# Performance work log

Hardware: AMD Instinct MI355X
Metric: run time of the kernel (lower is better)

## Reference

```python
import jax, jax.numpy as jnp
import numpy as np
from jax import lax

D_MODEL = 192; PATCH = 16; CH = 3
D_INNER = 384; D_STATE = 16; D_CONV = 4; DT_RANK = 12  # mamba_ssm defaults: expand=2, dt_rank=ceil(d_model/16)


def setup_inputs() -> dict:
    key = jax.random.key(0)
    ks = jax.random.split(key, 12)
    f32 = jnp.float32
    def rn(k, shape, s=0.02):
        return jax.random.normal(k, shape, f32) * s
    return {
        "x": jax.random.uniform(ks[0], (8, 3, 512, 512), f32),
        "patch_w": rn(ks[1], (D_MODEL, CH, PATCH, PATCH)),
        "patch_b": jnp.zeros((D_MODEL,), f32),
        "in_proj_w": rn(ks[2], (2 * D_INNER, D_MODEL)),
        "conv1d_w": rn(ks[3], (D_INNER, 1, D_CONV)),
        "conv1d_b": jnp.zeros((D_INNER,), f32),
        "x_proj_w": rn(ks[4], (DT_RANK + 2 * D_STATE, D_INNER)),
        "dt_proj_w": rn(ks[5], (D_INNER, DT_RANK)),
        "dt_proj_b": rn(ks[6], (D_INNER,), 0.1),
        "A_log": jnp.log(jnp.broadcast_to(jnp.arange(1, D_STATE + 1, dtype=f32), (D_INNER, D_STATE))),
        "D": jnp.ones((D_INNER,), f32),
        "out_proj_w": rn(ks[7], (D_MODEL, D_INNER)),
        "deconv_w": rn(ks[8], (D_MODEL, 64, PATCH, PATCH)),
        "deconv_b": jnp.zeros((64,), f32),
        "dec_conv_w": rn(ks[9], (CH, 64, 3, 3)),
        "dec_conv_b": jnp.zeros((CH,), f32),
    }


def _mamba(seq, in_proj_w, conv1d_w, conv1d_b, x_proj_w, dt_proj_w, dt_proj_b, A_log, D, out_proj_w):
    # seq: (B, L, d_model)
    B, L, _ = seq.shape
    xz = seq @ in_proj_w.T                              # (B, L, 2*d_inner)
    u, z = jnp.split(xz, 2, axis=-1)
    # depthwise causal conv1d (torch pads d_conv-1 both sides then truncates to L == left-pad only)
    uc = lax.conv_general_dilated(u.transpose(0, 2, 1), conv1d_w, (1,), [(D_CONV - 1, 0)],
                                  dimension_numbers=('NCH', 'OIH', 'NCH'),
                                  feature_group_count=D_INNER)       # (B, d_inner, L)
    u = jax.nn.silu((uc + conv1d_b[:, None]).transpose(0, 2, 1))     # (B, L, d_inner)
    dbc = u @ x_proj_w.T                                              # (B, L, dt_rank + 2*d_state)
    dt, Bm, Cm = jnp.split(dbc, [DT_RANK, DT_RANK + D_STATE], axis=-1)
    delta = jax.nn.softplus(dt @ dt_proj_w.T + dt_proj_b)            # (B, L, d_inner)
    A = -jnp.exp(A_log)                                               # (d_inner, d_state)
    dA = jnp.exp(delta[..., None] * A)                                # (B, L, d_inner, d_state)
    dBu = delta[..., None] * Bm[:, :, None, :] * u[..., None]         # (B, L, d_inner, d_state)
    def step(h, inp):
        a, b = inp
        h = a * h + b
        return h, h
    h0 = jnp.zeros((B, D_INNER, D_STATE), seq.dtype)
    _, hs = lax.scan(step, h0, (dA.transpose(1, 0, 2, 3), dBu.transpose(1, 0, 2, 3)))
    y = jnp.einsum('lbdn,bln->bld', hs, Cm) + u * D                   # (B, L, d_inner)
    y = y * jax.nn.silu(z)
    return y @ out_proj_w.T                                           # (B, L, d_model)


def reference(x, patch_w, patch_b, in_proj_w, conv1d_w, conv1d_b, x_proj_w,
              dt_proj_w, dt_proj_b, A_log, D, out_proj_w,
              deconv_w, deconv_b, dec_conv_w, dec_conv_b):
    B = x.shape[0]
    e = lax.conv_general_dilated(x, patch_w, (PATCH, PATCH), 'VALID',
                                 dimension_numbers=('NCHW', 'OIHW', 'NCHW')) + patch_b[:, None, None]
    h, w = e.shape[2], e.shape[3]
    seq = e.reshape(B, D_MODEL, h * w).transpose(0, 2, 1)             # (B, L, d_model)
    seq = _mamba(seq, in_proj_w, conv1d_w, conv1d_b, x_proj_w, dt_proj_w, dt_proj_b, A_log, D, out_proj_w)
    g = seq.transpose(0, 2, 1).reshape(B, D_MODEL, h, w)
    # ConvTranspose2d with stride == kernel_size is a non-overlapping patch expansion
    d = jnp.einsum('bchw,cdpq->bdhpwq', g, deconv_w).reshape(B, 64, h * PATCH, w * PATCH)
    d = jax.nn.relu(d + deconv_b[:, None, None])
    out = lax.conv_general_dilated(d, dec_conv_w, (1, 1), [(1, 1), (1, 1)],
                                   dimension_numbers=('NCHW', 'OIHW', 'NCHW')) + dec_conv_b[:, None, None]
    return jax.nn.sigmoid(out)
```

## Files before the change

kernel.cpp:

```cpp
#include <hip/hip_runtime.h>
#include <math.h>


typedef short bf16x8 __attribute__((ext_vector_type(8)));
typedef float f32x4 __attribute__((ext_vector_type(4)));

__device__ inline unsigned short f2bf(float f) {
    unsigned int u = __float_as_uint(f);
    unsigned int r = (u + 0x7fff + ((u >> 16) & 1)) >> 16;
    return (unsigned short)r;
}
__device__ inline float bf2f(unsigned short s) {
    return __uint_as_float(((unsigned int)s) << 16);
}

__global__ __launch_bounds__(256) void gemm_mfma_flex(
    const unsigned short* __restrict__ A, const unsigned short* __restrict__ W,
    void* __restrict__ Cout, const float* __restrict__ bias,
    int M, int N, int K, int out_bf16)
{
    __shared__ unsigned short As[128][48];
    __shared__ unsigned short Bs[128][48];
    const int tid = threadIdx.x;
    const int wave = tid >> 6, lane = tid & 63;
    const int wm = (wave & 1) * 64, wn = (wave >> 1) * 64;
    const int m0 = blockIdx.y * 128, n0 = blockIdx.x * 128;
    const int quad = lane >> 4, lr = lane & 15;
    const uint4 z4 = {0, 0, 0, 0};

    f32x4 acc[4][4];
    #pragma unroll
    for (int i = 0; i < 4; ++i)
        #pragma unroll
        for (int j = 0; j < 4; ++j)
            acc[i][j] = (f32x4){0.f, 0.f, 0.f, 0.f};

    const int r = tid >> 2, kq = tid & 3;
    for (int k0 = 0; k0 < K; k0 += 32) {
        #pragma unroll
        for (int half = 0; half < 2; ++half) {
            int rr = r + half * 64;
            *(uint4*)(&As[rr][kq * 8]) =
                *(const uint4*)(A + (size_t)(m0 + rr) * K + k0 + kq * 8);
            uint4 bv = z4;
            if (n0 + rr < N)
                bv = *(const uint4*)(W + (size_t)(n0 + rr) * K + k0 + kq * 8);
            *(uint4*)(&Bs[rr][kq * 8]) = bv;
        }
        __syncthreads();
        bf16x8 af[4], bfr[4];
        #pragma unroll
        for (int i = 0; i < 4; ++i) af[i] = *(const bf16x8*)(&As[wm + i * 16 + lr][quad * 8]);
        #pragma unroll
        for (int j = 0; j < 4; ++j) bfr[j] = *(const bf16x8*)(&Bs[wn + j * 16 + lr][quad * 8]);
        #pragma unroll
        for (int i = 0; i < 4; ++i)
            #pragma unroll
            for (int j = 0; j < 4; ++j)
                acc[i][j] = __builtin_amdgcn_mfma_f32_16x16x32_bf16(af[i], bfr[j], acc[i][j], 0, 0, 0);
        __syncthreads();
    }

    #pragma unroll
    for (int i = 0; i < 4; ++i) {
        int gm = m0 + wm + i * 16 + quad * 4;
        #pragma unroll
        for (int j = 0; j < 4; ++j) {
            int gn = n0 + wn + j * 16 + lr;
            if (gn >= N) continue;
            float bv = bias ? bias[gn] : 0.f;
            #pragma unroll
            for (int rr = 0; rr < 4; ++rr) {
                float v = acc[i][j][rr] + bv;
                if (out_bf16) ((unsigned short*)Cout)[(size_t)(gm + rr) * N + gn] = f2bf(v);
                else          ((float*)Cout)[(size_t)(gm + rr) * N + gn] = v;
            }
        }
    }
}

__global__ __launch_bounds__(256) void gemm_xd(
    const unsigned short* __restrict__ A, const unsigned short* __restrict__ W,
    float* __restrict__ delta, float* __restrict__ bc,
    const float* __restrict__ dtb)
{
    __shared__ unsigned short As[128][48];
    __shared__ unsigned short Bs[128][48];
    const int N = 416, K = 384;
    const int tid = threadIdx.x;
    const int wave = tid >> 6, lane = tid & 63;
    const int wm = (wave & 1) * 64, wn = (wave >> 1) * 64;
    const int m0 = blockIdx.y * 128, n0 = blockIdx.x * 128;
    const int quad = lane >> 4, lr = lane & 15;
    const uint4 z4 = {0, 0, 0, 0};

    f32x4 acc[4][4];
    #pragma unroll
    for (int i = 0; i < 4; ++i)
        #pragma unroll
        for (int j = 0; j < 4; ++j)
            acc[i][j] = (f32x4){0.f, 0.f, 0.f, 0.f};

    const int r = tid >> 2, kq = tid & 3;
    for (int k0 = 0; k0 < K; k0 += 32) {
        #pragma unroll
        for (int half = 0; half < 2; ++half) {
            int rr = r + half * 64;
            *(uint4*)(&As[rr][kq * 8]) =
                *(const uint4*)(A + (size_t)(m0 + rr) * K + k0 + kq * 8);
            uint4 bv = z4;
            if (n0 + rr < N)
                bv = *(const uint4*)(W + (size_t)(n0 + rr) * K + k0 + kq * 8);
            *(uint4*)(&Bs[rr][kq * 8]) = bv;
        }
        __syncthreads();
        bf16x8 af[4], bfr[4];
        #pragma unroll
        for (int i = 0; i < 4; ++i) af[i] = *(const bf16x8*)(&As[wm + i * 16 + lr][quad * 8]);
        #pragma unroll
        for (int j = 0; j < 4; ++j) bfr[j] = *(const bf16x8*)(&Bs[wn + j * 16 + lr][quad * 8]);
        #pragma unroll
        for (int i = 0; i < 4; ++i)
            #pragma unroll
            for (int j = 0; j < 4; ++j)
                acc[i][j] = __builtin_amdgcn_mfma_f32_16x16x32_bf16(af[i], bfr[j], acc[i][j], 0, 0, 0);
        __syncthreads();
    }

    #pragma unroll
    for (int i = 0; i < 4; ++i) {
        int gm = m0 + wm + i * 16 + quad * 4;
        #pragma unroll
        for (int j = 0; j < 4; ++j) {
            int gn = n0 + wn + j * 16 + lr;
            if (gn >= N) continue;
            #pragma unroll
            for (int rr = 0; rr < 4; ++rr) {
                float v = acc[i][j][rr];
                if (gn < 384) {
                    v += dtb[gn];
                    v = (v > 20.f) ? v : log1pf(__expf(v));
                    delta[(size_t)(gm + rr) * 384 + gn] = v;
                } else {
                    bc[(size_t)(gm + rr) * 32 + gn - 384] = v;
                }
            }
        }
    }
}

__global__ __launch_bounds__(256) void gemm_mfma_relu_bf16(
    const unsigned short* __restrict__ A0, const unsigned short* __restrict__ W,
    unsigned short* __restrict__ C0, const float* __restrict__ bias, int base_b)
{
    __shared__ unsigned short smem[12288];
    unsigned short* As = smem;
    unsigned short* Bs = smem + 6144;
    const int N = 16384, K = 192;
    const int tid = threadIdx.x;
    const int wave = tid >> 6, lane = tid & 63;
    const int wm = (wave & 1) * 64, wn = (wave >> 1) * 64;
    const int m0 = blockIdx.y * 128, n0 = blockIdx.x * 128;
    const int z = blockIdx.z;
    const unsigned short* A = A0 + (size_t)(base_b + z) * 1024 * 192;
    unsigned short* C = C0 + (size_t)z * 16777216;
    const int quad = lane >> 4, lr = lane & 15;

    f32x4 acc[4][4];
    #pragma unroll
    for (int i = 0; i < 4; ++i)
        #pragma unroll
        for (int j = 0; j < 4; ++j)
            acc[i][j] = (f32x4){0.f, 0.f, 0.f, 0.f};

    const int r = tid >> 2, kq = tid & 3;
    for (int k0 = 0; k0 < K; k0 += 32) {
        #pragma unroll
        for (int half = 0; half < 2; ++half) {
            int rr = r + half * 64;
            *(uint4*)(&As[rr * 48 + kq * 8]) =
                *(const uint4*)(A + (size_t)(m0 + rr) * K + k0 + kq * 8);
            *(uint4*)(&Bs[rr * 48 + kq * 8]) =
                *(const uint4*)(W + (size_t)(n0 + rr) * K + k0 + kq * 8);
        }
        __syncthreads();
        bf16x8 af[4], bfr[4];
        #pragma unroll
        for (int i = 0; i < 4; ++i) af[i] = *(const bf16x8*)(&As[(wm + i * 16 + lr) * 48 + quad * 8]);
        #pragma unroll
        for (int j = 0; j < 4; ++j) bfr[j] = *(const bf16x8*)(&Bs[(wn + j * 16 + lr) * 48 + quad * 8]);
        #pragma unroll
        for (int i = 0; i < 4; ++i)
            #pragma unroll
            for (int j = 0; j < 4; ++j)
                acc[i][j] = __builtin_amdgcn_mfma_f32_16x16x32_bf16(af[i], bfr[j], acc[i][j], 0, 0, 0);
        __syncthreads();
    }

    unsigned short* Ct = smem;
    #pragma unroll
    for (int h = 0; h < 2; ++h) {
        if ((wave & 1) == h) {
            #pragma unroll
            for (int i = 0; i < 4; ++i) {
                int lrow = i * 16 + quad * 4;
                #pragma unroll
                for (int j = 0; j < 4; ++j) {
                    int lcol = wn + j * 16 + lr;
                    float bv = bias[(n0 + lcol) & 63];
                    #pragma unroll
                    for (int rr = 0; rr < 4; ++rr) {
                        float v = fmaxf(acc[i][j][rr] + bv, 0.f);
                        Ct[(lrow + rr) * 136 + lcol] = f2bf(v);
                    }
                }
            }
        }
        __syncthreads();
        #pragma unroll
        for (int p = 0; p < 4; ++p) {
            int idx = p * 256 + tid;
            int row = idx >> 4, cg = idx & 15;
            *(uint4*)(C + (size_t)(m0 + h * 64 + row) * N + n0 + cg * 8) =
                *(const uint4*)(&Ct[row * 136 + cg * 8]);
        }
        __syncthreads();
    }
}

__global__ __launch_bounds__(256) void prep_all(
    const float* __restrict__ x, unsigned short* __restrict__ P,
    const float* __restrict__ patch_w, unsigned short* __restrict__ wp,
    const float* __restrict__ in_proj_w, unsigned short* __restrict__ wi,
    const float* __restrict__ out_proj_w, unsigned short* __restrict__ wo,
    const float* __restrict__ deconv_w, unsigned short* __restrict__ W2,
    const float* __restrict__ dec_conv_w, unsigned short* __restrict__ wconv,
    const float* __restrict__ dtw, const float* __restrict__ xpw,
    unsigned short* __restrict__ wxd)
{
    int i = blockIdx.x * 256 + threadIdx.x;
    if (i < 6291456) {
        int col = i % 768, row = i / 768;
        int b = row >> 10, l = row & 1023;
        int h = l >> 5, w = l & 31;
        int c = col >> 8, p = (col >> 4) & 15, q = col & 15;
        P[i] = f2bf(x[((size_t)(b * 3 + c) * 512 + (h * 16 + p)) * 512 + (w * 16 + q)]);
        return;
    }
    i -= 6291456;
    if (i < 147456) { wp[i] = f2bf(patch_w[i]); return; }
    i -= 147456;
    if (i < 147456) { wi[i] = f2bf(in_proj_w[i]); return; }
    i -= 147456;
    if (i < 73728) { wo[i] = f2bf(out_proj_w[i]); return; }
    i -= 73728;
    if (i < 3145728) {
        int c = i % 192, np = i / 192;
        int k = np & 63, pq = np >> 6;
        W2[i] = f2bf(deconv_w[(size_t)c * 16384 + k * 256 + pq]);
        return;
    }
    i -= 3145728;
    if (i < 9216) {
        int ch = i & 63, m = (i >> 6) & 15, tap = i >> 10;
        int dy = tap / 3, dx = tap % 3;
        float v = (m < 3) ? dec_conv_w[((m * 64 + ch) * 3 + dy) * 3 + dx] : 0.f;
        wconv[i] = f2bf(v);
        return;
    }
    i -= 9216;
    {
        int col = i % 384, row = i / 384;
        float v;
        if (row < 384) {
            v = 0.f;
            #pragma unroll
            for (int j = 0; j < 12; ++j)
                v = fmaf(dtw[row * 12 + j], xpw[j * 384 + col], v);
        } else {
            v = xpw[(row - 384 + 12) * 384 + col];
        }
        wxd[i] = f2bf(v);
    }
}

__global__ __launch_bounds__(256) void conv1d_silu(const unsigned short* __restrict__ xz,
                                                   const float* __restrict__ cw,
                                                   const float* __restrict__ cb,
                                                   float* __restrict__ u32,
                                                   unsigned short* __restrict__ u16)
{
    int idx = blockIdx.x * 256 + threadIdx.x;
    int d = idx % 384;
    int row = idx / 384;
    int l = row & 1023;
    float acc = cb[d];
    #pragma unroll
    for (int j = 0; j < 4; ++j) {
        int ll = l - 3 + j;
        if (ll >= 0) acc += bf2f(xz[(size_t)(row - 3 + j) * 768 + d]) * cw[d * 4 + j];
    }
    float s = acc / (1.f + __expf(-acc));
    u32[idx] = s;
    u16[idx] = f2bf(s);
}

__global__ __launch_bounds__(256) void ssm_pass1(const float* __restrict__ delta,
                                                 const float* __restrict__ bc,
                                                 const float* __restrict__ u,
                                                 const float* __restrict__ A_log,
                                                 float* __restrict__ Pc,
                                                 float* __restrict__ Hc)
{
    const int tid = threadIdx.x;
    const int n4 = tid & 3, dloc = tid >> 2;
    const int c = blockIdx.x, dg = blockIdx.y, b = blockIdx.z;
    const int d = dg * 64 + dloc;
    const int blk = (b * 6 + dg) * 32 + c;
    f32x4 A4 = *(const f32x4*)(A_log + d * 16 + n4 * 4);
    float Aa[4];
    #pragma unroll
    for (int j = 0; j < 4; ++j) Aa[j] = -__expf(A4[j]);
    const float* dp = delta + (size_t)(b * 1024) * 384 + d;
    const float* up = u     + (size_t)(b * 1024) * 384 + d;
    const float* bp = bc    + (size_t)(b * 1024) * 32;
    float P[4] = {1.f, 1.f, 1.f, 1.f}, H[4] = {0.f, 0.f, 0.f, 0.f};
    const int l0 = c * 32;
    for (int l = l0; l < l0 + 32; ++l) {
        float dlv = dp[(size_t)l * 384];
        float ulv = up[(size_t)l * 384];
        f32x4 B4 = *(const f32x4*)(bp + (size_t)l * 32 + n4 * 4);
        float du = dlv * ulv;
        #pragma unroll
        for (int j = 0; j < 4; ++j) {
            float a = __expf(dlv * Aa[j]);
            P[j] *= a;
            H[j] = fmaf(a, H[j], du * B4[j]);
        }
    }
    size_t o = ((size_t)blk * 256 + tid) * 4;
    *(f32x4*)(Pc + o) = (f32x4){P[0], P[1], P[2], P[3]};
    *(f32x4*)(Hc + o) = (f32x4){H[0], H[1], H[2], H[3]};
}

__global__ __launch_bounds__(256) void ssm_pass2(const float* __restrict__ Pc,
                                                 const float* __restrict__ Hc,
                                                 float* __restrict__ h0c)
{
    int t = blockIdx.x * 256 + threadIdx.x;
    int grp = t >> 10, dn = t & 1023;
    float h = 0.f;
    #pragma unroll
    for (int c = 0; c < 32; ++c) {
        size_t idx = ((size_t)(grp * 32 + c)) * 1024 + dn;
        h0c[idx] = h;
        h = fmaf(Pc[idx], h, Hc[idx]);
    }
}

__global__ __launch_bounds__(256) void ssm_pass3(const float* __restrict__ delta,
                                                 const float* __restrict__ bc,
                                                 const float* __restrict__ u,
                                                 const unsigned short* __restrict__ xz,
                                                 const float* __restrict__ A_log,
                                                 const float* __restrict__ Dp,
                                                 const float* __restrict__ h0c,
                                                 unsigned short* __restrict__ y16)
{
    const int tid = threadIdx.x;
    const int n4 = tid & 3, dloc = tid >> 2;
    const int c = blockIdx.x, dg = blockIdx.y, b = blockIdx.z;
    const int d = dg * 64 + dloc;
    const int blk = (b * 6 + dg) * 32 + c;
    f32x4 A4 = *(const f32x4*)(A_log + d * 16 + n4 * 4);
    float Aa[4];
    #pragma unroll
    for (int j = 0; j < 4; ++j) Aa[j] = -__expf(A4[j]);
    float Dv = Dp[d];
    const float* dp = delta + (size_t)(b * 1024) * 384 + d;
    const float* up = u     + (size_t)(b * 1024) * 384 + d;
    const float* bp = bc    + (size_t)(b * 1024) * 32;
    const unsigned short* zp = xz + (size_t)(b * 1024) * 768 + 384 + d;
    unsigned short* yp = y16 + (size_t)(b * 1024) * 384 + d;
    f32x4 h4 = *(const f32x4*)(h0c + ((size_t)blk * 256 + tid) * 4);
    float H[4] = {h4[0], h4[1], h4[2], h4[3]};
    const int l0 = c * 32;
    for (int l = l0; l < l0 + 32; ++l) {
        float dlv = dp[(size_t)l * 384];
        float ulv = up[(size_t)l * 384];
        f32x4 B4 = *(const f32x4*)(bp + (size_t)l * 32 + n4 * 4);
        f32x4 C4 = *(const f32x4*)(bp + (size_t)l * 32 + 16 + n4 * 4);
        float du = dlv * ulv;
        float part = 0.f;
        #pragma unroll
        for (int j = 0; j < 4; ++j) {
            float a = __expf(dlv * Aa[j]);
            H[j] = fmaf(a, H[j], du * B4[j]);
            part = fmaf(H[j], C4[j], part);
        }
        part += __shfl_xor(part, 1, 4);
        part += __shfl_xor(part, 2, 4);
        if (n4 == 0) {
            float z = bf2f(zp[(size_t)l * 768]);
            float sz = z / (1.f + __expf(-z));
            yp[(size_t)l * 384] = f2bf((part + ulv * Dv) * sz);
        }
    }
}

__global__ __launch_bounds__(256) void decconv_mfma(
    const unsigned short* __restrict__ Db, const unsigned short* __restrict__ wconv,
    const float* __restrict__ dcb, float* __restrict__ out, int base_b)
{
    __shared__ unsigned short ds[18 * 18 * 72];
    const int t = threadIdx.x;
    const int pidx = blockIdx.x;
    const int bb = blockIdx.y;
    const int b = base_b + bb;
    const unsigned short* Dbb = Db + (size_t)bb * 16777216;
    const int ph = pidx >> 5, pw = pidx & 31;
    const uint4 z4 = {0, 0, 0, 0};

    const unsigned short* base = Dbb + ((size_t)pidx << 14);
    #pragma unroll
    for (int s = 0; s < 8; ++s) {
        int f = s * 256 + t;
        int k8 = f & 7, pq = f >> 3;
        *(uint4*)&ds[(((pq >> 4) + 1) * 18 + (pq & 15) + 1) * 72 + k8 * 8] =
            *(const uint4*)(base + pq * 64 + k8 * 8);
    }
    {
        int k8 = t & 7, e = (t >> 3) & 15;
        if (t < 128) {
            uint4 v = z4;
            if (ph > 0) v = *(const uint4*)(Dbb + ((size_t)(pidx - 32) << 14) + (240 + e) * 64 + k8 * 8);
            *(uint4*)&ds[(0 * 18 + e + 1) * 72 + k8 * 8] = v;
        } else {
            uint4 v = z4;
            if (ph < 31) v = *(const uint4*)(Dbb + ((size_t)(pidx + 32) << 14) + e * 64 + k8 * 8);
            *(uint4*)&ds[(17 * 18 + e + 1) * 72 + k8 * 8] = v;
        }
        if (t < 128) {
            uint4 v = z4;
            if (pw > 0) v = *(const uint4*)(Dbb + ((size_t)(pidx - 1) << 14) + (e * 16 + 15) * 64 + k8 * 8);
            *(uint4*)&ds[((e + 1) * 18 + 0) * 72 + k8 * 8] = v;
        } else {
            uint4 v = z4;
            if (pw < 31) v = *(const uint4*)(Dbb + ((size_t)(pidx + 1) << 14) + (e * 16) * 64 + k8 * 8);
            *(uint4*)&ds[((e + 1) * 18 + 17) * 72 + k8 * 8] = v;
        }
        if (t < 32) {
            int c = t >> 3;
            int dh = (c >> 1) * 2 - 1, dw = (c & 1) * 2 - 1;
            int nh = ph + dh, nw = pw + dw;
            int sp = dh < 0 ? 15 : 0, sq = dw < 0 ? 15 : 0;
            uint4 v = z4;
            if (nh >= 0 && nh < 32 && nw >= 0 && nw < 32)
                v = *(const uint4*)(Dbb + ((size_t)(nh * 32 + nw) << 14) + (sp * 16 + sq) * 64 + k8 * 8);
            int dy = dh < 0 ? 0 : 17, dx = dw < 0 ? 0 : 17;
            *(uint4*)&ds[(dy * 18 + dx) * 72 + k8 * 8] = v;
        }
    }
    __syncthreads();

    const int wave = t >> 6, lane = t & 63;
    const int quad = lane >> 4, lr = lane & 15;
    f32x4 acc[4];
    #pragma unroll
    for (int i = 0; i < 4; ++i) acc[i] = (f32x4){0.f, 0.f, 0.f, 0.f};

    #pragma unroll
    for (int tap = 0; tap < 9; ++tap) {
        const int dy = tap / 3, dx = tap % 3;
        bf16x8 a0 = *(const bf16x8*)(wconv + (tap * 16 + lr) * 64 + quad * 8);
        bf16x8 a1 = *(const bf16x8*)(wconv + (tap * 16 + lr) * 64 + 32 + quad * 8);
        #pragma unroll
        for (int i = 0; i < 4; ++i) {
            int p = wave * 4 + i;
            const unsigned short* cell = &ds[((p + dy) * 18 + lr + dx) * 72];
            bf16x8 b0 = *(const bf16x8*)(cell + quad * 8);
            bf16x8 b1 = *(const bf16x8*)(cell + 32 + quad * 8);
            acc[i] = __builtin_amdgcn_mfma_f32_16x16x32_bf16(a0, b0, acc[i], 0, 0, 0);
            acc[i] = __builtin_amdgcn_mfma_f32_16x16x32_bf16(a1, b1, acc[i], 0, 0, 0);
        }
    }

    if (quad == 0) {
        float b0 = dcb[0], b1 = dcb[1], b2 = dcb[2];
        #pragma unroll
        for (int i = 0; i < 4; ++i) {
            int Y = ph * 16 + wave * 4 + i, X = pw * 16 + lr;
            size_t o = (size_t)(b * 3) * 262144 + (size_t)Y * 512 + X;
            out[o]          = 1.f / (1.f + __expf(-(acc[i][0] + b0)));
            out[o + 262144] = 1.f / (1.f + __expf(-(acc[i][1] + b1)));
            out[o + 524288] = 1.f / (1.f + __expf(-(acc[i][2] + b2)));
        }
    }
}

#define WS_P16      0
#define WS_DELTA    0
#define WS_SEQ16    3145728
#define WS_XZ16     3538944
#define WS_U32      6684672
#define WS_U16      9830400
#define WS_Y16      9830400
#define WS_BC       10223616
#define WS_PC       10485760
#define WS_HC       12058624
#define WS_H0C      13631488

extern "C" void kernel_launch(void* const* d_in, const int* in_sizes, int n_in,
                              void* d_out, int out_size, void* d_ws, size_t ws_size,
                              hipStream_t stream)
{
    const float* x         = (const float*)d_in[0];
    const float* patch_w   = (const float*)d_in[1];
    const float* patch_b   = (const float*)d_in[2];
    const float* in_proj_w = (const float*)d_in[3];
    const float* conv1d_w  = (const float*)d_in[4];
    const float* conv1d_b  = (const float*)d_in[5];
    const float* x_proj_w  = (const float*)d_in[6];
    const float* dt_proj_w = (const float*)d_in[7];
    const float* dt_proj_b = (const float*)d_in[8];
    const float* A_log     = (const float*)d_in[9];
    const float* Dp        = (const float*)d_in[10];
    const float* out_proj_w= (const float*)d_in[11];
    const float* deconv_w  = (const float*)d_in[12];
    const float* deconv_b  = (const float*)d_in[13];
    const float* dec_conv_w= (const float*)d_in[14];
    const float* dec_conv_b= (const float*)d_in[15];
    float* out = (float*)d_out;
    float* ws  = (float*)d_ws;

    const int G = (ws_size >= (size_t)143157248) ? 4 : 2;
    const size_t wbase = (G == 4) ? 33554432 : 16777216;

    unsigned short* P16   = (unsigned short*)(ws + WS_P16);
    float*          delta = ws + WS_DELTA;
    unsigned short* seq16 = (unsigned short*)(ws + WS_SEQ16);
    unsigned short* xz16  = (unsigned short*)(ws + WS_XZ16);
    float*          u32   = ws + WS_U32;
    unsigned short* u16   = (unsigned short*)(ws + WS_U16);
    unsigned short* y16   = (unsigned short*)(ws + WS_Y16);
    float*          bc    = ws + WS_BC;
    float*          Pc    = ws + WS_PC;
    float*          Hc    = ws + WS_HC;
    float*          h0c   = ws + WS_H0C;
    unsigned short* Db16  = (unsigned short*)(ws);
    unsigned short* seqo_b= (unsigned short*)(ws + wbase);
    unsigned short* W2b   = (unsigned short*)(ws + wbase + 393216);
    unsigned short* wconv = (unsigned short*)(ws + wbase + 1966080);
    unsigned short* wp16  = (unsigned short*)(ws + wbase + 1970688);
    unsigned short* wi16  = (unsigned short*)(ws + wbase + 2044416);
    unsigned short* wo16  = (unsigned short*)(ws + wbase + 2118144);
    unsigned short* wxd   = (unsigned short*)(ws + wbase + 2155008);

    prep_all<<<38964, 256, 0, stream>>>(x, P16, patch_w, wp16, in_proj_w, wi16,
                                        out_proj_w, wo16, deconv_w, W2b,
                                        dec_conv_w, wconv, dt_proj_w, x_proj_w, wxd);
    gemm_mfma_flex<<<dim3(2, 64), 256, 0, stream>>>(P16, wp16, seq16, patch_b,
                                                    8192, 192, 768, 1);
    gemm_mfma_flex<<<dim3(6, 64), 256, 0, stream>>>(seq16, wi16, xz16, nullptr,
                                                    8192, 768, 192, 1);
    conv1d_silu<<<12288, 256, 0, stream>>>(xz16, conv1d_w, conv1d_b, u32, u16);
    gemm_xd<<<dim3(4, 64), 256, 0, stream>>>(u16, wxd, delta, bc, dt_proj_b);
    ssm_pass1<<<dim3(32, 6, 8), 256, 0, stream>>>(delta, bc, u32, A_log, Pc, Hc);
    ssm_pass2<<<192, 256, 0, stream>>>(Pc, Hc, h0c);
    ssm_pass3<<<dim3(32, 6, 8), 256, 0, stream>>>(delta, bc, u32, xz16, A_log, Dp, h0c, y16);
    gemm_mfma_flex<<<dim3(2, 64), 256, 0, stream>>>(y16, wo16, seqo_b, nullptr,
                                                    8192, 192, 384, 1);
    for (int g = 0; g < 8 / G; ++g) {
        gemm_mfma_relu_bf16<<<dim3(128, 8, G), 256, 0, stream>>>(
            seqo_b, W2b, Db16, deconv_b, g * G);
        decconv_mfma<<<dim3(1024, G), 256, 0, stream>>>(Db16, wconv, dec_conv_b, out, g * G);
    }
}
```

Baseline: 535.1 us.

## Drop fp32 SSM input copy, shrink LDS row padding, fix group size to four

The conv1d kernel no longer writes an fp32 copy of the activated input; both SSM passes now read the bf16 copy and widen it, cutting write and read traffic. The LDS row stride in the GEMM kernels drops from 48 to 40 halves, which shrinks shared memory and changes the bank-conflict pattern of the fragment reads. The workspace layout is repacked and the deconv batch group is hard-coded to 4, removing the fallback for smaller workspaces. Using the rounded bf16 value in the scan adds a little precision loss.

```diff
diff --git a/kernel.cpp b/kernel.cpp
--- a/kernel.cpp
+++ b/kernel.cpp
@@ -19,8 +19,8 @@
     void* __restrict__ Cout, const float* __restrict__ bias,
     int M, int N, int K, int out_bf16)
 {
-    __shared__ unsigned short As[128][48];
-    __shared__ unsigned short Bs[128][48];
+    __shared__ unsigned short As[128][40];
+    __shared__ unsigned short Bs[128][40];
     const int tid = threadIdx.x;
     const int wave = tid >> 6, lane = tid & 63;
     const int wm = (wave & 1) * 64, wn = (wave >> 1) * 64;
@@ -84,8 +84,8 @@
     float* __restrict__ delta, float* __restrict__ bc,
     const float* __restrict__ dtb)
 {
-    __shared__ unsigned short As[128][48];
-    __shared__ unsigned short Bs[128][48];
+    __shared__ unsigned short As[128][40];
+    __shared__ unsigned short Bs[128][40];
     const int N = 416, K = 384;
     const int tid = threadIdx.x;
     const int wave = tid >> 6, lane = tid & 63;
@@ -153,9 +153,9 @@
     const unsigned short* __restrict__ A0, const unsigned short* __restrict__ W,
     unsigned short* __restrict__ C0, const float* __restrict__ bias, int base_b)
 {
-    __shared__ unsigned short smem[12288];
+    __shared__ unsigned short smem[10240];
     unsigned short* As = smem;
-    unsigned short* Bs = smem + 6144;
+    unsigned short* Bs = smem + 5120;
     const int N = 16384, K = 192;
     const int tid = threadIdx.x;
     const int wave = tid >> 6, lane = tid & 63;
@@ -178,17 +178,17 @@
         #pragma unroll
         for (int half = 0; half < 2; ++half) {
             int rr = r + half * 64;
-            *(uint4*)(&As[rr * 48 + kq * 8]) =
+            *(uint4*)(&As[rr * 40 + kq * 8]) =
                 *(const uint4*)(A + (size_t)(m0 + rr) * K + k0 + kq * 8);
-            *(uint4*)(&Bs[rr * 48 + kq * 8]) =
+            *(uint4*)(&Bs[rr * 40 + kq * 8]) =
                 *(const uint4*)(W + (size_t)(n0 + rr) * K + k0 + kq * 8);
         }
         __syncthreads();
         bf16x8 af[4], bfr[4];
         #pragma unroll
-        for (int i = 0; i < 4; ++i) af[i] = *(const bf16x8*)(&As[(wm + i * 16 + lr) * 48 + quad * 8]);
-        #pragma unroll
-        for (int j = 0; j < 4; ++j) bfr[j] = *(const bf16x8*)(&Bs[(wn + j * 16 + lr) * 48 + quad * 8]);
+        for (int i = 0; i < 4; ++i) af[i] = *(const bf16x8*)(&As[(wm + i * 16 + lr) * 40 + quad * 8]);
+        #pragma unroll
+        for (int j = 0; j < 4; ++j) bfr[j] = *(const bf16x8*)(&Bs[(wn + j * 16 + lr) * 40 + quad * 8]);
         #pragma unroll
         for (int i = 0; i < 4; ++i)
             #pragma unroll
@@ -287,7 +287,6 @@
 __global__ __launch_bounds__(256) void conv1d_silu(const unsigned short* __restrict__ xz,
                                                    const float* __restrict__ cw,
                                                    const float* __restrict__ cb,
-                                                   float* __restrict__ u32,
                                                    unsigned short* __restrict__ u16)
 {
     int idx = blockIdx.x * 256 + threadIdx.x;
@@ -301,13 +300,12 @@
         if (ll >= 0) acc += bf2f(xz[(size_t)(row - 3 + j) * 768 + d]) * cw[d * 4 + j];
     }
     float s = acc / (1.f + __expf(-acc));
-    u32[idx] = s;
     u16[idx] = f2bf(s);
 }
 
 __global__ __launch_bounds__(256) void ssm_pass1(const float* __restrict__ delta,
                                                  const float* __restrict__ bc,
-                                                 const float* __restrict__ u,
+                                                 const unsigned short* __restrict__ u,
                                                  const float* __restrict__ A_log,
                                                  float* __restrict__ Pc,
                                                  float* __restrict__ Hc)
@@ -322,13 +320,13 @@
     #pragma unroll
     for (int j = 0; j < 4; ++j) Aa[j] = -__expf(A4[j]);
     const float* dp = delta + (size_t)(b * 1024) * 384 + d;
-    const float* up = u     + (size_t)(b * 1024) * 384 + d;
+    const unsigned short* up = u + (size_t)(b * 1024) * 384 + d;
     const float* bp = bc    + (size_t)(b * 1024) * 32;
     float P[4] = {1.f, 1.f, 1.f, 1.f}, H[4] = {0.f, 0.f, 0.f, 0.f};
     const int l0 = c * 32;
     for (int l = l0; l < l0 + 32; ++l) {
         float dlv = dp[(size_t)l * 384];
-        float ulv = up[(size_t)l * 384];
+        float ulv = bf2f(up[(size_t)l * 384]);
         f32x4 B4 = *(const f32x4*)(bp + (size_t)l * 32 + n4 * 4);
         float du = dlv * ulv;
         #pragma unroll
@@ -360,7 +358,7 @@
 
 __global__ __launch_bounds__(256) void ssm_pass3(const float* __restrict__ delta,
                                                  const float* __restrict__ bc,
-                                                 const float* __restrict__ u,
+                                                 const unsigned short* __restrict__ u,
                                                  const unsigned short* __restrict__ xz,
                                                  const float* __restrict__ A_log,
                                                  const float* __restrict__ Dp,
@@ -378,7 +376,7 @@
     for (int j = 0; j < 4; ++j) Aa[j] = -__expf(A4[j]);
     float Dv = Dp[d];
     const float* dp = delta + (size_t)(b * 1024) * 384 + d;
-    const float* up = u     + (size_t)(b * 1024) * 384 + d;
+    const unsigned short* up = u + (size_t)(b * 1024) * 384 + d;
     const float* bp = bc    + (size_t)(b * 1024) * 32;
     const unsigned short* zp = xz + (size_t)(b * 1024) * 768 + 384 + d;
     unsigned short* yp = y16 + (size_t)(b * 1024) * 384 + d;
@@ -387,7 +385,7 @@
     const int l0 = c * 32;
     for (int l = l0; l < l0 + 32; ++l) {
         float dlv = dp[(size_t)l * 384];
-        float ulv = up[(size_t)l * 384];
+        float ulv = bf2f(up[(size_t)l * 384]);
         f32x4 B4 = *(const f32x4*)(bp + (size_t)l * 32 + n4 * 4);
         f32x4 C4 = *(const f32x4*)(bp + (size_t)l * 32 + 16 + n4 * 4);
         float du = dlv * ulv;
@@ -498,17 +496,16 @@
     }
 }
 
-#define WS_P16      0
 #define WS_DELTA    0
 #define WS_SEQ16    3145728
-#define WS_XZ16     3538944
-#define WS_U32      6684672
-#define WS_U16      9830400
-#define WS_Y16      9830400
+#define WS_XZ16     3932160
+#define WS_U16      7077888
+#define WS_Y16      8650752
 #define WS_BC       10223616
 #define WS_PC       10485760
 #define WS_HC       12058624
 #define WS_H0C      13631488
+#define WS_WBASE    33554432
 
 extern "C" void kernel_launch(void* const* d_in, const int* in_sizes, int n_in,
                               void* d_out, int out_size, void* d_ws, size_t ws_size,
@@ -533,14 +530,10 @@
     float* out = (float*)d_out;
     float* ws  = (float*)d_ws;
 
-    const int G = (ws_size >= (size_t)143157248) ? 4 : 2;
-    const size_t wbase = (G == 4) ? 33554432 : 16777216;
-
-    unsigned short* P16   = (unsigned short*)(ws + WS_P16);
+    unsigned short* P16   = (unsigned short*)(ws + WS_DELTA);
     float*          delta = ws + WS_DELTA;
     unsigned short* seq16 = (unsigned short*)(ws + WS_SEQ16);
     unsigned short* xz16  = (unsigned short*)(ws + WS_XZ16);
-    float*          u32   = ws + WS_U32;
     unsigned short* u16   = (unsigned short*)(ws + WS_U16);
     unsigned short* y16   = (unsigned short*)(ws + WS_Y16);
     float*          bc    = ws + WS_BC;
@@ -548,13 +541,13 @@
     float*          Hc    = ws + WS_HC;
     float*          h0c   = ws + WS_H0C;
     unsigned short* Db16  = (unsigned short*)(ws);
-    unsigned short* seqo_b= (unsigned short*)(ws + wbase);
-    unsigned short* W2b   = (unsigned short*)(ws + wbase + 393216);
-    unsigned short* wconv = (unsigned short*)(ws + wbase + 1966080);
-    unsigned short* wp16  = (unsigned short*)(ws + wbase + 1970688);
-    unsigned short* wi16  = (unsigned short*)(ws + wbase + 2044416);
-    unsigned short* wo16  = (unsigned short*)(ws + wbase + 2118144);
-    unsigned short* wxd   = (unsigned short*)(ws + wbase + 2155008);
+    unsigned short* seqo_b= (unsigned short*)(ws + WS_WBASE);
+    unsigned short* W2b   = (unsigned short*)(ws + WS_WBASE + 786432);
+    unsigned short* wconv = (unsigned short*)(ws + WS_WBASE + 2359296);
+    unsigned short* wp16  = (unsigned short*)(ws + WS_WBASE + 2361600);
+    unsigned short* wi16  = (unsigned short*)(ws + WS_WBASE + 2435328);
+    unsigned short* wo16  = (unsigned short*)(ws + WS_WBASE + 2509056);
+    unsigned short* wxd   = (unsigned short*)(ws + WS_WBASE + 2545920);
 
     prep_all<<<38964, 256, 0, stream>>>(x, P16, patch_w, wp16, in_proj_w, wi16,
                                         out_proj_w, wo16, deconv_w, W2b,
@@ -563,16 +556,16 @@
                                                     8192, 192, 768, 1);
     gemm_mfma_flex<<<dim3(6, 64), 256, 0, stream>>>(seq16, wi16, xz16, nullptr,
                                                     8192, 768, 192, 1);
-    conv1d_silu<<<12288, 256, 0, stream>>>(xz16, conv1d_w, conv1d_b, u32, u16);
+    conv1d_silu<<<12288, 256, 0, stream>>>(xz16, conv1d_w, conv1d_b, u16);
     gemm_xd<<<dim3(4, 64), 256, 0, stream>>>(u16, wxd, delta, bc, dt_proj_b);
-    ssm_pass1<<<dim3(32, 6, 8), 256, 0, stream>>>(delta, bc, u32, A_log, Pc, Hc);
+    ssm_pass1<<<dim3(32, 6, 8), 256, 0, stream>>>(delta, bc, u16, A_log, Pc, Hc);
     ssm_pass2<<<192, 256, 0, stream>>>(Pc, Hc, h0c);
-    ssm_pass3<<<dim3(32, 6, 8), 256, 0, stream>>>(delta, bc, u32, xz16, A_log, Dp, h0c, y16);
+    ssm_pass3<<<dim3(32, 6, 8), 256, 0, stream>>>(delta, bc, u16, xz16, A_log, Dp, h0c, y16);
     gemm_mfma_flex<<<dim3(2, 64), 256, 0, stream>>>(y16, wo16, seqo_b, nullptr,
                                                     8192, 192, 384, 1);
-    for (int g = 0; g < 8 / G; ++g) {
-        gemm_mfma_relu_bf16<<<dim3(128, 8, G), 256, 0, stream>>>(
-            seqo_b, W2b, Db16, deconv_b, g * G);
-        decconv_mfma<<<dim3(1024, G), 256, 0, stream>>>(Db16, wconv, dec_conv_b, out, g * G);
-    }
-}
+    for (int g = 0; g < 2; ++g) {
+        gemm_mfma_relu_bf16<<<dim3(128, 8, 4), 256, 0, stream>>>(
+            seqo_b, W2b, Db16, deconv_b, g * 4);
+        decconv_mfma<<<dim3(1024, 4), 256, 0, stream>>>(Db16, wconv, dec_conv_b, out, g * 4);
+    }
+}
```

New measurement: 538.0 us. Within noise of the previous version (+0.5%).
